# Kernel tuning notes

Measured on AMD Instinct MI355X. Metric: run time of the kernel, lower is better.

Reference implementation:

```python
import jax, jax.numpy as jnp
import numpy as np

DIM = 100
SAMPLE = 12
NEG = -9e15
LRELU = 0.2  # opt.alpha


def _forward(emb, pos_table, w1, w2, glu1_w, glu2_w, glu2_b,
             a0, a1, a2, a3, gw1, gw2, gw3, num_w, mask_item,
             alias_inputs, adj, items, seq_features, adj_all):
    B, L = items.shape
    h = emb[items]  # [B, L, D]

    # ---- LocalAggregator: e_k[b,i,j] = leaky_relu(sum_d h[b,i,d]*h[b,j,d]*a_k[d])
    # (same math as tiling to [B, N*N, D] then matmul with a_k, without the huge intermediate)
    def rel(a):
        return jax.nn.leaky_relu(jnp.einsum('bid,bjd->bij', h, h * a[:, 0]), LRELU)

    alpha = jnp.full((B, L, L), NEG, dtype=h.dtype)
    for k, a in enumerate((a0, a1, a2, a3)):
        alpha = jnp.where(adj == k + 1, rel(a), alpha)
    alpha = jax.nn.softmax(alpha, axis=-1)
    h_local = jnp.einsum('bij,bjd->bid', alpha, h)

    # ---- Global: sample 1-hop neighbors from adj_all / num tables
    nbr_idx = adj_all[items]          # [B, L, S]
    nbr_w = num_w[items]              # [B, L, S]
    nbr_vec = emb[nbr_idx]            # [B, L, S, D]

    # session info (mean of masked seq-feature embeddings)
    item_emb = emb[seq_features] * mask_item[..., None]
    sess = jnp.sum(item_emb, axis=1) / jnp.sum(mask_item, axis=-1, keepdims=True)  # [B, D]
    sess = jnp.broadcast_to(sess[:, None, :], (B, L, DIM))

    # GlobalAggregator with extra_vector
    a_in = jnp.concatenate([sess[:, :, None, :] * nbr_vec, nbr_w[..., None]], axis=-1)  # [B,L,S,D+1]
    att = jax.nn.leaky_relu(a_in @ gw1, LRELU)          # [B, L, S, D]
    att = jax.nn.softmax((att @ gw2)[..., 0], axis=-1)  # [B, L, S]
    agg = jnp.sum(att[..., None] * nbr_vec, axis=-2)    # [B, L, D]
    h_global = jax.nn.relu(jnp.concatenate([h, agg], axis=-1) @ gw3)

    h_comb = h_local + h_global
    seq_hidden = jnp.take_along_axis(h_comb, alias_inputs[..., None], axis=1)  # [B, L, D]

    rmask = mask_item[..., None]
    pos = jnp.broadcast_to(pos_table[:L][None], seq_hidden.shape)
    hs = jnp.sum(seq_hidden * rmask, axis=1) / jnp.sum(rmask, axis=1)  # [B, D]
    nh = jnp.tanh(jnp.concatenate([pos, seq_hidden], axis=-1) @ w1)
    nh = jax.nn.sigmoid(nh @ glu1_w + (hs @ glu2_w + glu2_b)[:, None, :])
    beta = (nh @ w2) * rmask                 # [B, L, 1]
    select = jnp.sum(beta * seq_hidden, 1)   # [B, D]
    score = select @ emb[1:].T               # skip item id 0 (padding)
    return jax.nn.softmax(score, axis=-1)


def setup_inputs():
    key = jax.random.key(0)
    B, L, NN, S, D = 256, 64, 100000, SAMPLE, DIM
    stdv = 1.0 / np.sqrt(D)
    ks = jax.random.split(key, 24)
    u = lambda k, s: jax.random.uniform(k, s, jnp.float32, -stdv, stdv)
    return {
        'emb': u(ks[0], (NN, D)),
        'pos_table': u(ks[1], (200, D)),
        'w1': u(ks[2], (2 * D, D)),
        'w2': u(ks[3], (D, 1)),
        'glu1_w': u(ks[4], (D, D)),
        'glu2_w': u(ks[5], (D, D)),
        'glu2_b': u(ks[6], (D,)),
        'a0': u(ks[7], (D, 1)),
        'a1': u(ks[8], (D, 1)),
        'a2': u(ks[9], (D, 1)),
        'a3': u(ks[10], (D, 1)),
        'gw1': u(ks[11], (D + 1, D)),
        'gw2': u(ks[12], (D, 1)),
        'gw3': u(ks[13], (2 * D, D)),
        'num_w': jax.random.uniform(ks[14], (NN, S), jnp.float32, 0.0, 1.0),
        'mask_item': jnp.ones((B, L), jnp.float32),
        'alias_inputs': jax.random.randint(ks[15], (B, L), 0, L),
        'adj': jax.random.randint(ks[16], (B, L, L), 0, 5),
        'items': jax.random.randint(ks[17], (B, L), 0, NN),
        'seq_features': jax.random.randint(ks[18], (B, L), 0, NN),
        'adj_all': jax.random.randint(ks[19], (NN, S), 0, NN),
    }


def reference(emb, pos_table, w1, w2, glu1_w, glu2_w, glu2_b, a0, a1, a2, a3,
              gw1, gw2, gw3, num_w, mask_item, alias_inputs, adj, items,
              seq_features, adj_all):
    return _forward(emb, pos_table, w1, w2, glu1_w, glu2_w, glu2_b,
                    a0, a1, a2, a3, gw1, gw2, gw3, num_w, mask_item,
                    alias_inputs, adj, items, seq_features, adj_all)
```

## Files before the change

kernel.cpp:

```cpp
#include <hip/hip_runtime.h>
#include <math.h>

#define B 256
#define L 64
#define D 100
#define S 12
#define NN 100000
#define E 99999
#define NEG -9e15f
#define LRELU 0.2f
#define M3A (B*L*S)
#define NT5 782
#define CH 28

__device__ __forceinline__ float lrelu(float x){ return x > 0.f ? x : LRELU*x; }

__global__ void k0_pos(const float* __restrict__ pos, const float* __restrict__ w1,
                       float* __restrict__ pos_part){
    int l = blockIdx.x; int d = threadIdx.x;
    if (d >= D) return;
    float acc = 0.f;
    for (int c = 0; c < D; ++c) acc += pos[l*D+c] * w1[c*D+d];
    pos_part[l*D+d] = acc;
}

__global__ void k1_gather(const float* __restrict__ emb, const int* __restrict__ items,
                          const int* __restrict__ seqf, const float* __restrict__ mask,
                          float* __restrict__ h, float* __restrict__ sess){
    int b = blockIdx.x; int tid = threadIdx.x;
    for (int e = tid; e < L*25; e += blockDim.x){
        int l = e / 25, q = e % 25;
        *(float4*)&h[(long)(b*L+l)*D + q*4] =
            *(const float4*)&emb[(long)items[b*L+l]*D + q*4];
    }
    if (tid < D){
        float acc = 0.f, msum = 0.f;
        for (int l = 0; l < L; ++l){
            float mk = mask[b*L+l];
            acc  += emb[(long)seqf[b*L+l]*D + tid] * mk;
            msum += mk;
        }
        sess[b*D+tid] = acc / msum;
    }
}

__global__ __launch_bounds__(256) void k2_local(const float* __restrict__ h,
                         const int* __restrict__ adj,
                         const float* __restrict__ a0, const float* __restrict__ a1,
                         const float* __restrict__ a2, const float* __restrict__ a3,
                         float* __restrict__ hcomb){
    __shared__ __align__(16) float Hd[L*132];
    __shared__ float Alr[L*66];
    __shared__ __align__(16) float a4s[D*4];
    int tid = threadIdx.x;
    int tx = tid & 15, ty = tid >> 4;
    int b = blockIdx.x;

    for (int t = tid; t < D; t += 256){
        a4s[t*4+0] = a0[t]; a4s[t*4+1] = a1[t]; a4s[t*4+2] = a2[t]; a4s[t*4+3] = a3[t];
    }
    for (int e = tid; e < L*D; e += 256){
        int i = e / D, d = e - i*D;
        Hd[i*132 + d] = h[(long)(b*L+i)*D + d];
    }
    for (int e = tid; e < L*32; e += 256){
        int i = e >> 5, c = D + (e & 31);
        Hd[i*132 + c] = 0.f;
    }
    __syncthreads();

    int ksel[4][4];
    #pragma unroll
    for (int i=0;i<4;++i)
        #pragma unroll
        for (int j=0;j<4;++j)
            ksel[i][j] = adj[((long)b*L + ty*4+i)*L + tx*4+j];

    float e0[4][4]={}, e1[4][4]={}, e2[4][4]={}, e3[4][4]={};
    for (int d = 0; d < D; ++d){
        float4 aw = *(const float4*)&a4s[d*4];
        float hi[4], hj[4];
        #pragma unroll
        for (int i=0;i<4;++i) hi[i] = Hd[(ty*4+i)*132 + d];
        #pragma unroll
        for (int j=0;j<4;++j) hj[j] = Hd[(tx*4+j)*132 + d];
        #pragma unroll
        for (int i=0;i<4;++i)
            #pragma unroll
            for (int j=0;j<4;++j){
                float p = hi[i]*hj[j];
                e0[i][j] += p*aw.x;
                e1[i][j] += p*aw.y;
                e2[i][j] += p*aw.z;
                e3[i][j] += p*aw.w;
            }
    }

    #pragma unroll
    for (int i=0;i<4;++i){
        float s[4];
        #pragma unroll
        for (int j=0;j<4;++j){
            int k = ksel[i][j];
            float ev = (k==1) ? e0[i][j] : (k==2) ? e1[i][j]
                     : (k==3) ? e2[i][j] : e3[i][j];
            s[j] = (k>=1 && k<=4) ? lrelu(ev) : NEG;
        }
        float m = fmaxf(fmaxf(s[0],s[1]), fmaxf(s[2],s[3]));
        #pragma unroll
        for (int off=1; off<16; off<<=1) m = fmaxf(m, __shfl_xor(m, off));
        float es[4], sum = 0.f;
        #pragma unroll
        for (int j=0;j<4;++j){ es[j] = expf(s[j]-m); sum += es[j]; }
        #pragma unroll
        for (int off=1; off<16; off<<=1) sum += __shfl_xor(sum, off);
        float inv = 1.f/sum;
        #pragma unroll
        for (int j=0;j<4;++j) Alr[(ty*4+i)*66 + tx*4+j] = es[j]*inv;
    }
    __syncthreads();

    float o[4][8];
    #pragma unroll
    for (int i=0;i<4;++i)
        #pragma unroll
        for (int jj=0;jj<8;++jj) o[i][jj] = 0.f;
    for (int j = 0; j < L; ++j){
        float al[4];
        #pragma unroll
        for (int i=0;i<4;++i) al[i] = Alr[(ty*4+i)*66 + j];
        float4 b0 = *(const float4*)&Hd[j*132 + tx*4];
        float4 b1 = *(const float4*)&Hd[j*132 + 64 + tx*4];
        float bv[8] = {b0.x,b0.y,b0.z,b0.w,b1.x,b1.y,b1.z,b1.w};
        #pragma unroll
        for (int i=0;i<4;++i)
            #pragma unroll
            for (int jj=0;jj<8;++jj) o[i][jj] += al[i]*bv[jj];
    }
    #pragma unroll
    for (int i=0;i<4;++i){
        int row = ty*4+i;
        #pragma unroll
        for (int jj=0;jj<8;++jj){
            int d = (jj<4) ? (tx*4+jj) : (64 + tx*4 + (jj-4));
            if (d < D) hcomb[(long)(b*L+row)*D + d] = o[i][jj];
        }
    }
}

__global__ __launch_bounds__(256) void k3a_logits(const float* __restrict__ emb,
                          const float* __restrict__ sess,
                          const int* __restrict__ items, const int* __restrict__ adj_all,
                          const float* __restrict__ num_w,
                          const float* __restrict__ gw1, const float* __restrict__ gw2,
                          float* __restrict__ att_l){
    __shared__ __align__(16) float As[CH*128];
    __shared__ __align__(16) float Bs[CH*128];
    __shared__ int   idxr[128];
    __shared__ float nbwr[128];
    int tid = threadIdx.x;
    int tx = tid & 15, ty = tid >> 4;
    int r0 = blockIdx.x * 128;
    int b  = r0 / (L*S);

    if (tid < 128){
        int r = r0 + tid;
        int bl = r / S, s = r - bl*S;
        int it = items[bl];
        idxr[tid] = adj_all[it*S + s];
        nbwr[tid] = num_w[it*S + s];
    }
    __syncthreads();

    float acc[8][8];
    #pragma unroll
    for (int i=0;i<8;++i)
        #pragma unroll
        for (int j=0;j<8;++j) acc[i][j] = 0.f;

    for (int chunk = 0; chunk < 4; ++chunk){
        int c0 = chunk*CH;
        for (int e = tid; e < 128*7; e += 256){
            int rl = e & 127, cq = e >> 7;
            int cb = c0 + cq*4;
            float vx=0.f, vy=0.f, vz=0.f, vw=0.f;
            if (cb < D){
                const float4 v  = *(const float4*)&emb[(long)idxr[rl]*D + cb];
                const float4 sv = *(const float4*)&sess[(long)b*D + cb];
                vx = v.x*sv.x; vy = v.y*sv.y; vz = v.z*sv.z; vw = v.w*sv.w;
            } else if (cb == D){
                vx = nbwr[rl];
            }
            As[(cq*4+0)*128 + rl] = vx;
            As[(cq*4+1)*128 + rl] = vy;
            As[(cq*4+2)*128 + rl] = vz;
            As[(cq*4+3)*128 + rl] = vw;
        }
        for (int e = tid; e < CH*128; e += 256){
            int d = e & 127, cc = e >> 7;
            int c = c0 + cc;
            Bs[cc*128 + d] = (c <= D && d < D) ? gw1[c*D + d] : 0.f;
        }
        __syncthreads();
        for (int k = 0; k < CH; ++k){
            float4 a0v = *(const float4*)&As[k*128 + ty*8];
            float4 a1v = *(const float4*)&As[k*128 + ty*8 + 4];
            float4 b0 = *(const float4*)&Bs[k*128 + tx*4];
            float4 b1 = *(const float4*)&Bs[k*128 + 64 + tx*4];
            float av[8] = {a0v.x,a0v.y,a0v.z,a0v.w,a1v.x,a1v.y,a1v.z,a1v.w};
            float bv[8] = {b0.x,b0.y,b0.z,b0.w,b1.x,b1.y,b1.z,b1.w};
            #pragma unroll
            for (int i=0;i<8;++i)
                #pragma unroll
                for (int j=0;j<8;++j) acc[i][j] += av[i]*bv[j];
        }
        __syncthreads();
    }
    float g[8];
    #pragma unroll
    for (int j=0;j<8;++j){
        int d = (j<4) ? (tx*4+j) : (64 + tx*4 + (j-4));
        g[j] = (d < D) ? gw2[d] : 0.f;
    }
    #pragma unroll
    for (int i=0;i<8;++i){
        float p = 0.f;
        #pragma unroll
        for (int j=0;j<8;++j) p += lrelu(acc[i][j]) * g[j];
        #pragma unroll
        for (int off=1; off<16; off<<=1) p += __shfl_xor(p, off);
        if (tx == 0) att_l[r0 + ty*8 + i] = p;
    }
}

__global__ __launch_bounds__(256) void k3b_agg(const float* __restrict__ emb,
                          const int* __restrict__ items, const int* __restrict__ adj_all,
                          const float* __restrict__ att_l,
                          float* __restrict__ agg){
    int p = blockIdx.x*2 + (threadIdx.x >> 7);
    int t = threadIdx.x & 127;
    float lg[S];
    float m = -INFINITY;
    #pragma unroll
    for (int s=0;s<S;++s){ lg[s] = att_l[p*S + s]; m = fmaxf(m, lg[s]); }
    float sum = 0.f;
    #pragma unroll
    for (int s=0;s<S;++s){ lg[s] = expf(lg[s]-m); sum += lg[s]; }
    float inv = 1.f/sum;
    if (t < D){
        int it = items[p];
        float acc = 0.f;
        #pragma unroll
        for (int s=0;s<S;++s){
            int idx = adj_all[it*S + s];
            acc += lg[s]*inv * emb[(long)idx*D + t];
        }
        agg[p*D + t] = acc;
    }
}

__global__ __launch_bounds__(256) void k3c_hg(const float* __restrict__ h,
                          const float* __restrict__ agg, const float* __restrict__ gw3,
                          float* __restrict__ hcomb){
    __shared__ __align__(16) float As[52*64];
    __shared__ __align__(16) float Bs[52*128];
    int tid = threadIdx.x;
    int tx = tid & 15, ty = tid >> 4;
    int r0 = blockIdx.x * 64;

    float acc[4][8];
    #pragma unroll
    for (int i=0;i<4;++i)
        #pragma unroll
        for (int j=0;j<8;++j) acc[i][j] = 0.f;

    for (int chunk = 0; chunk < 4; ++chunk){
        int c0 = chunk*52;
        for (int e = tid; e < 64*13; e += 256){
            int rl = e & 63, cq = e >> 6;
            int cb = c0 + cq*4;
            float4 v = {0.f,0.f,0.f,0.f};
            if (cb < D)            v = *(const float4*)&h[(long)(r0+rl)*D + cb];
            else if (cb < 2*D)     v = *(const float4*)&agg[(long)(r0+rl)*D + (cb-D)];
            As[(cq*4+0)*64 + rl] = v.x;
            As[(cq*4+1)*64 + rl] = v.y;
            As[(cq*4+2)*64 + rl] = v.z;
            As[(cq*4+3)*64 + rl] = v.w;
        }
        for (int e = tid; e < 52*128; e += 256){
            int d = e & 127, cc = e >> 7;
            int c = c0 + cc;
            Bs[cc*128 + d] = (c < 2*D && d < D) ? gw3[c*D + d] : 0.f;
        }
        __syncthreads();
        for (int k = 0; k < 52; ++k){
            float4 a  = *(const float4*)&As[k*64 + ty*4];
            float4 b0 = *(const float4*)&Bs[k*128 + tx*4];
            float4 b1 = *(const float4*)&Bs[k*128 + 64 + tx*4];
            float av[4] = {a.x,a.y,a.z,a.w};
            float bv[8] = {b0.x,b0.y,b0.z,b0.w,b1.x,b1.y,b1.z,b1.w};
            #pragma unroll
            for (int i=0;i<4;++i)
                #pragma unroll
                for (int j=0;j<8;++j) acc[i][j] += av[i]*bv[j];
        }
        __syncthreads();
    }
    #pragma unroll
    for (int i=0;i<4;++i){
        int r = r0 + ty*4 + i;
        #pragma unroll
        for (int j=0;j<8;++j){
            int d = (j<4) ? (tx*4+j) : (64 + tx*4 + (j-4));
            if (d < D){
                long o = (long)r*D + d;
                hcomb[o] += fmaxf(acc[i][j], 0.f);
            }
        }
    }
}

__global__ __launch_bounds__(128) void k4a_gate(const float* __restrict__ hcomb,
                          const int* __restrict__ alias_in, const float* __restrict__ mask,
                          const float* __restrict__ glu2_w, const float* __restrict__ glu2_b,
                          float* __restrict__ gate){
    int b = blockIdx.x; int tid = threadIdx.x;
    __shared__ float hsl[D];
    __shared__ float mkl[L];
    __shared__ int   al[L];
    if (tid < L){ al[tid] = alias_in[b*L+tid]; mkl[tid] = mask[b*L+tid]; }
    __syncthreads();
    if (tid < D){
        float acc = 0.f, msum = 0.f;
        for (int l = 0; l < L; ++l){
            acc  += hcomb[(long)(b*L + al[l])*D + tid] * mkl[l];
            msum += mkl[l];
        }
        hsl[tid] = acc / msum;
    }
    __syncthreads();
    if (tid < D){
        float g = glu2_b[tid];
        for (int c = 0; c < D; ++c) g += hsl[c]*glu2_w[c*D+tid];
        gate[b*D+tid] = g;
    }
}

__global__ __launch_bounds__(256) void k4b_nh1(const float* __restrict__ hcomb,
                          const int* __restrict__ alias_in,
                          const float* __restrict__ w1, const float* __restrict__ pos_part,
                          float* __restrict__ nh1){
    __shared__ __align__(16) float As[52*64];
    __shared__ __align__(16) float Bs[52*128];
    __shared__ int al[64];
    int tid = threadIdx.x;
    int tx = tid & 15, ty = tid >> 4;
    int b = blockIdx.x;
    int r0 = b * 64;

    if (tid < 64) al[tid] = alias_in[r0 + tid];
    __syncthreads();

    float acc[4][8];
    #pragma unroll
    for (int i=0;i<4;++i)
        #pragma unroll
        for (int j=0;j<8;++j) acc[i][j] = 0.f;

    for (int chunk = 0; chunk < 2; ++chunk){
        int c0 = chunk*52;
        for (int e = tid; e < 64*13; e += 256){
            int rl = e & 63, cq = e >> 6;
            int cb = c0 + cq*4;
            float4 v = {0.f,0.f,0.f,0.f};
            if (cb < D) v = *(const float4*)&hcomb[(long)(r0 + al[rl])*D + cb];
            As[(cq*4+0)*64 + rl] = v.x;
            As[(cq*4+1)*64 + rl] = v.y;
            As[(cq*4+2)*64 + rl] = v.z;
            As[(cq*4+3)*64 + rl] = v.w;
        }
        for (int e = tid; e < 52*128; e += 256){
            int d = e & 127, cc = e >> 7;
            int c = c0 + cc;
            Bs[cc*128 + d] = (c < D && d < D) ? w1[(D+c)*D + d] : 0.f;
        }
        __syncthreads();
        for (int k = 0; k < 52; ++k){
            float4 a  = *(const float4*)&As[k*64 + ty*4];
            float4 b0 = *(const float4*)&Bs[k*128 + tx*4];
            float4 b1 = *(const float4*)&Bs[k*128 + 64 + tx*4];
            float av[4] = {a.x,a.y,a.z,a.w};
            float bv[8] = {b0.x,b0.y,b0.z,b0.w,b1.x,b1.y,b1.z,b1.w};
            #pragma unroll
            for (int i=0;i<4;++i)
                #pragma unroll
                for (int j=0;j<8;++j) acc[i][j] += av[i]*bv[j];
        }
        __syncthreads();
    }
    #pragma unroll
    for (int i=0;i<4;++i){
        int rl = ty*4 + i;
        #pragma unroll
        for (int j=0;j<8;++j){
            int d = (j<4) ? (tx*4+j) : (64 + tx*4 + (j-4));
            if (d < D){
                float v = tanhf(acc[i][j] + pos_part[rl*D + d]);
                nh1[(long)(r0+rl)*D + d] = v;
            }
        }
    }
}

__global__ __launch_bounds__(256) void k4c_select(const float* __restrict__ nh1,
                          const float* __restrict__ hcomb, const int* __restrict__ alias_in,
                          const float* __restrict__ glu1_w, const float* __restrict__ gate,
                          const float* __restrict__ w2, const float* __restrict__ mask,
                          float* __restrict__ sel_out){
    __shared__ __align__(16) float As[104*64];
    __shared__ __align__(16) float Bs[52*128];
    __shared__ __align__(16) float Ss[64*D];
    __shared__ float red[16*128];
    __shared__ float w2l[128];
    __shared__ float mkl[64];
    __shared__ int   al[64];
    int tid = threadIdx.x;
    int tx = tid & 15, ty = tid >> 4;
    int b = blockIdx.x;
    int r0 = b * 64;

    if (tid < 64){ al[tid] = alias_in[r0 + tid]; mkl[tid] = mask[r0 + tid]; }
    if (tid < 128) w2l[tid] = (tid < D) ? w2[tid] : 0.f;
    __syncthreads();

    for (int e = tid; e < 64*26; e += 256){
        int rl = e & 63, cq = e >> 6;
        int cb = cq*4;
        float4 v = {0.f,0.f,0.f,0.f};
        if (cb < D) v = *(const float4*)&nh1[(long)(r0+rl)*D + cb];
        As[(cb+0)*64 + rl] = v.x;
        As[(cb+1)*64 + rl] = v.y;
        As[(cb+2)*64 + rl] = v.z;
        As[(cb+3)*64 + rl] = v.w;
    }
    for (int e = tid; e < 64*25; e += 256){
        int rl = e / 25, q = e % 25;
        *(float4*)&Ss[rl*D + q*4] = *(const float4*)&hcomb[(long)(r0 + al[rl])*D + q*4];
    }

    float acc[4][8];
    #pragma unroll
    for (int i=0;i<4;++i)
        #pragma unroll
        for (int j=0;j<8;++j) acc[i][j] = 0.f;

    for (int chunk = 0; chunk < 2; ++chunk){
        int c0 = chunk*52;
        __syncthreads();
        for (int e = tid; e < 52*128; e += 256){
            int d = e & 127, cc = e >> 7;
            int c = c0 + cc;
            Bs[cc*128 + d] = (c < D && d < D) ? glu1_w[c*D + d] : 0.f;
        }
        __syncthreads();
        for (int k = 0; k < 52; ++k){
            float4 a  = *(const float4*)&As[(c0+k)*64 + ty*4];
            float4 b0 = *(const float4*)&Bs[k*128 + tx*4];
            float4 b1 = *(const float4*)&Bs[k*128 + 64 + tx*4];
            float av[4] = {a.x,a.y,a.z,a.w};
            float bv[8] = {b0.x,b0.y,b0.z,b0.w,b1.x,b1.y,b1.z,b1.w};
            #pragma unroll
            for (int i=0;i<4;++i)
                #pragma unroll
                for (int j=0;j<8;++j) acc[i][j] += av[i]*bv[j];
        }
    }
    __syncthreads();

    float gl[8];
    #pragma unroll
    for (int j=0;j<8;++j){
        int d = (j<4) ? (tx*4+j) : (64 + tx*4 + (j-4));
        gl[j] = (d < D) ? gate[b*D + d] : 0.f;
    }
    float sp[8];
    #pragma unroll
    for (int j=0;j<8;++j) sp[j] = 0.f;
    #pragma unroll
    for (int i=0;i<4;++i){
        int rl = ty*4 + i;
        float p = 0.f;
        #pragma unroll
        for (int j=0;j<8;++j){
            int d = (j<4) ? (tx*4+j) : (64 + tx*4 + (j-4));
            float z = acc[i][j] + gl[j];
            float nh2 = 1.f/(1.f+expf(-z));
            p += nh2 * w2l[d];
        }
        #pragma unroll
        for (int off=1; off<16; off<<=1) p += __shfl_xor(p, off);
        float beta = p * mkl[rl];
        #pragma unroll
        for (int j=0;j<8;++j){
            int d = (j<4) ? (tx*4+j) : (64 + tx*4 + (j-4));
            if (d < D) sp[j] += beta * Ss[rl*D + d];
        }
    }
    #pragma unroll
    for (int j=0;j<8;++j){
        int d = (j<4) ? (tx*4+j) : (64 + tx*4 + (j-4));
        red[ty*128 + d] = sp[j];
    }
    __syncthreads();
    if (tid < 128){
        float s = 0.f;
        #pragma unroll
        for (int g=0; g<16; ++g) s += red[g*128 + tid];
        if (tid < D) sel_out[b*D + tid] = s;
    }
}

__global__ __launch_bounds__(256) void k5_score(const float* __restrict__ emb,
                                                const float* __restrict__ sel,
                                                float* __restrict__ out,
                                                float* __restrict__ pstats){
    __shared__ __align__(16) float As[CH*128];
    __shared__ __align__(16) float Bs[CH*128];
    int tid = threadIdx.x;
    int tx = tid & 15, ty = tid >> 4;
    int n0 = blockIdx.x * 128;
    int m0 = blockIdx.y * 128;

    float acc[8][8];
    #pragma unroll
    for (int i=0;i<8;++i)
        #pragma unroll
        for (int j=0;j<8;++j) acc[i][j] = 0.f;

    for (int chunk = 0; chunk < 4; ++chunk){
        int c0 = chunk*CH;
        for (int e = tid; e < 128*7; e += 256){
            int rl = e & 127, cq = e >> 7;
            int cb = c0 + cq*4;
            float4 v = {0.f,0.f,0.f,0.f};
            if (cb < D) v = *(const float4*)&sel[(long)(m0+rl)*D + cb];
            As[(cq*4+0)*128 + rl] = v.x;
            As[(cq*4+1)*128 + rl] = v.y;
            As[(cq*4+2)*128 + rl] = v.z;
            As[(cq*4+3)*128 + rl] = v.w;
        }
        for (int e = tid; e < 128*7; e += 256){
            int nl = e & 127, cq = e >> 7;
            int cb = c0 + cq*4;
            int n = n0 + nl;
            float4 v = {0.f,0.f,0.f,0.f};
            if (cb < D && n < E) v = *(const float4*)&emb[(long)(1+n)*D + cb];
            Bs[(cq*4+0)*128 + nl] = v.x;
            Bs[(cq*4+1)*128 + nl] = v.y;
            Bs[(cq*4+2)*128 + nl] = v.z;
            Bs[(cq*4+3)*128 + nl] = v.w;
        }
        __syncthreads();
        for (int k = 0; k < CH; ++k){
            float4 a0v = *(const float4*)&As[k*128 + ty*8];
            float4 a1v = *(const float4*)&As[k*128 + ty*8 + 4];
            float4 b0 = *(const float4*)&Bs[k*128 + tx*4];
            float4 b1 = *(const float4*)&Bs[k*128 + 64 + tx*4];
            float av[8] = {a0v.x,a0v.y,a0v.z,a0v.w,a1v.x,a1v.y,a1v.z,a1v.w};
            float bv[8] = {b0.x,b0.y,b0.z,b0.w,b1.x,b1.y,b1.z,b1.w};
            #pragma unroll
            for (int i=0;i<8;++i)
                #pragma unroll
                for (int j=0;j<8;++j) acc[i][j] += av[i]*bv[j];
        }
        __syncthreads();
    }
    bool fullTile = (n0 + 128 <= E);
    #pragma unroll
    for (int i=0;i<8;++i){
        int m = m0 + ty*8 + i;
        long rowo = (long)m*E;
        if (fullTile){
            *(float4*)&out[rowo + n0 + tx*4]      = *(float4*)&acc[i][0];
            *(float4*)&out[rowo + n0 + 64 + tx*4] = *(float4*)&acc[i][4];
        } else {
            #pragma unroll
            for (int j=0;j<8;++j){
                int n = n0 + ((j<4) ? (tx*4+j) : (64 + tx*4 + (j-4)));
                if (n < E) out[rowo + n] = acc[i][j];
            }
        }
        float mx = -INFINITY, sm = 0.f;
        #pragma unroll
        for (int j=0;j<8;++j){
            int n = n0 + ((j<4) ? (tx*4+j) : (64 + tx*4 + (j-4)));
            if (n < E){
                float v = acc[i][j];
                if (v > mx){ sm = sm*expf(mx - v) + 1.f; mx = v; }
                else         sm += expf(v - mx);
            }
        }
        #pragma unroll
        for (int off=1; off<16; off<<=1){
            float mo = __shfl_xor(mx, off);
            float so = __shfl_xor(sm, off);
            float mm = fmaxf(mx, mo);
            float sn = 0.f;
            if (mx > -INFINITY) sn += sm*expf(mx-mm);
            if (mo > -INFINITY) sn += so*expf(mo-mm);
            mx = mm; sm = sn;
        }
        if (tx == 0){
            long o = ((long)m*NT5 + blockIdx.x)*2;
            pstats[o] = mx; pstats[o+1] = sm;
        }
    }
}

__global__ __launch_bounds__(256) void k7_combine(const float* __restrict__ pstats,
                                                  float* __restrict__ MS){
    int row = blockIdx.x;
    int tid = threadIdx.x;
    float m = -INFINITY, s = 0.f;
    for (int t = tid; t < NT5; t += 256){
        long o = ((long)row*NT5 + t)*2;
        float m2 = pstats[o], s2 = pstats[o+1];
        float mm = fmaxf(m, m2);
        float sn = 0.f;
        if (m  > -INFINITY) sn += s *expf(m -mm);
        if (m2 > -INFINITY) sn += s2*expf(m2-mm);
        m = mm; s = sn;
    }
    __shared__ float ms[256], ss[256];
    ms[tid] = m; ss[tid] = s;
    __syncthreads();
    for (int off = 128; off >= 1; off >>= 1){
        if (tid < off){
            float m1 = ms[tid], s1 = ss[tid];
            float m2 = ms[tid+off], s2 = ss[tid+off];
            float mm = fmaxf(m1, m2);
            float sn = 0.f;
            if (m1 > -INFINITY) sn += s1*expf(m1-mm);
            if (m2 > -INFINITY) sn += s2*expf(m2-mm);
            ms[tid] = mm; ss[tid] = sn;
        }
        __syncthreads();
    }
    if (tid == 0){ MS[row*2] = ms[0]; MS[row*2+1] = 1.f/ss[0]; }
}

__global__ __launch_bounds__(256) void k8_norm(float* __restrict__ out,
                                               const float* __restrict__ MS){
    long base = ((long)blockIdx.x*256 + threadIdx.x)*4;
    const long total = (long)B*E;
    if (base < total){
        float4 v = *(float4*)&out[base];
        float r[4] = {v.x, v.y, v.z, v.w};
        #pragma unroll
        for (int c=0;c<4;++c){
            long el = base + c;
            int b = (int)(el / E);
            r[c] = expf(r[c] - MS[b*2]) * MS[b*2+1];
        }
        v.x = r[0]; v.y = r[1]; v.z = r[2]; v.w = r[3];
        *(float4*)&out[base] = v;
    }
}

extern "C" void kernel_launch(void* const* d_in, const int* in_sizes, int n_in,
                              void* d_out, int out_size, void* d_ws, size_t ws_size,
                              hipStream_t stream) {
    const float* emb       = (const float*)d_in[0];
    const float* pos_table = (const float*)d_in[1];
    const float* w1        = (const float*)d_in[2];
    const float* w2        = (const float*)d_in[3];
    const float* glu1_w    = (const float*)d_in[4];
    const float* glu2_w    = (const float*)d_in[5];
    const float* glu2_b    = (const float*)d_in[6];
    const float* a0        = (const float*)d_in[7];
    const float* a1        = (const float*)d_in[8];
    const float* a2        = (const float*)d_in[9];
    const float* a3        = (const float*)d_in[10];
    const float* gw1       = (const float*)d_in[11];
    const float* gw2       = (const float*)d_in[12];
    const float* gw3       = (const float*)d_in[13];
    const float* num_w     = (const float*)d_in[14];
    const float* mask      = (const float*)d_in[15];
    const int*   alias_in  = (const int*)d_in[16];
    const int*   adj       = (const int*)d_in[17];
    const int*   items     = (const int*)d_in[18];
    const int*   seqf      = (const int*)d_in[19];
    const int*   adj_all   = (const int*)d_in[20];

    float* ws       = (float*)d_ws;
    float* h        = ws;
    float* hcomb    = h + B*L*D;
    float* sess     = hcomb + B*L*D;
    float* pos_part = sess + B*D;
    float* sel      = pos_part + L*D;
    float* att_l    = sel + B*D;
    float* agg      = att_l + M3A;
    float* pstats   = agg + B*L*D;
    float* MS       = pstats + B*NT5*2;
    float* gate     = MS + B*2;
    float* nh1      = agg;

    float* out = (float*)d_out;

    k0_pos    <<<dim3(L), dim3(128), 0, stream>>>(pos_table, w1, pos_part);
    k1_gather <<<dim3(B), dim3(128), 0, stream>>>(emb, items, seqf, mask, h, sess);
    k2_local  <<<dim3(B), dim3(256), 0, stream>>>(h, adj, a0, a1, a2, a3, hcomb);
    k3a_logits<<<dim3(M3A/128), dim3(256), 0, stream>>>(emb, sess, items, adj_all, num_w,
                                                        gw1, gw2, att_l);
    k3b_agg   <<<dim3(B*L/2), dim3(256), 0, stream>>>(emb, items, adj_all, att_l, agg);
    k3c_hg    <<<dim3(B*L/64), dim3(256), 0, stream>>>(h, agg, gw3, hcomb);
    k4a_gate  <<<dim3(B), dim3(128), 0, stream>>>(hcomb, alias_in, mask, glu2_w, glu2_b, gate);
    k4b_nh1   <<<dim3(B), dim3(256), 0, stream>>>(hcomb, alias_in, w1, pos_part, nh1);
    k4c_select<<<dim3(B), dim3(256), 0, stream>>>(nh1, hcomb, alias_in, glu1_w, gate,
                                                  w2, mask, sel);
    k5_score  <<<dim3(NT5, 2), dim3(256), 0, stream>>>(emb, sel, out, pstats);
    k7_combine<<<dim3(B), dim3(256), 0, stream>>>(pstats, MS);
    k8_norm   <<<dim3((B*E/4 + 255)/256, 1), dim3(256), 0, stream>>>(out, MS);
}
```

Measured before the change: 622.7 us.

## Retile score GEMM to wide item tiles with transposed session vectors read directly

The k4c_select kernel now also writes a transposed, zero-padded copy of the session vectors. The score kernel reads A operands for its 8 rows straight from that copy in global memory (broadcast within a wavefront) instead of staging them in shared memory. Each block now covers 256 items × 32 rows with 8×4 register tiles, and the grid grows to 8 row blocks. The aim is to raise occupancy through smaller register and shared-memory footprints and to stream the 400MB output better. The cost is that each embedding tile is reloaded 8 times instead of twice, and A operands now come from global loads.

```diff
diff --git a/kernel.cpp b/kernel.cpp
--- a/kernel.cpp
+++ b/kernel.cpp
@@ -10,7 +10,7 @@
 #define NEG -9e15f
 #define LRELU 0.2f
 #define M3A (B*L*S)
-#define NT5 782
+#define NT5 391
 #define CH 28
 
 __device__ __forceinline__ float lrelu(float x){ return x > 0.f ? x : LRELU*x; }
@@ -416,7 +416,7 @@
                           const float* __restrict__ hcomb, const int* __restrict__ alias_in,
                           const float* __restrict__ glu1_w, const float* __restrict__ gate,
                           const float* __restrict__ w2, const float* __restrict__ mask,
-                          float* __restrict__ sel_out){
+                          float* __restrict__ sel_out, float* __restrict__ selT){
     __shared__ __align__(16) float As[104*64];
     __shared__ __align__(16) float Bs[52*128];
     __shared__ __align__(16) float Ss[64*D];
@@ -516,92 +516,81 @@
         float s = 0.f;
         #pragma unroll
         for (int g=0; g<16; ++g) s += red[g*128 + tid];
-        if (tid < D) sel_out[b*D + tid] = s;
+        if (tid < D){
+            sel_out[b*D + tid] = s;
+            selT[(long)tid*256 + b] = s;
+        } else if (tid < 112){
+            selT[(long)tid*256 + b] = 0.f;
+        }
     }
 }
 
 __global__ __launch_bounds__(256) void k5_score(const float* __restrict__ emb,
-                                                const float* __restrict__ sel,
+                                                const float* __restrict__ selT,
                                                 float* __restrict__ out,
                                                 float* __restrict__ pstats){
-    __shared__ __align__(16) float As[CH*128];
-    __shared__ __align__(16) float Bs[CH*128];
+    __shared__ __align__(16) float Bs[CH*256];
     int tid = threadIdx.x;
-    int tx = tid & 15, ty = tid >> 4;
-    int n0 = blockIdx.x * 128;
-    int m0 = blockIdx.y * 128;
-
-    float acc[8][8];
+    int wid = tid >> 6, lane = tid & 63;
+    int n0 = blockIdx.x * 256;
+    int r0 = blockIdx.y * 32 + wid * 8;
+
+    float acc[8][4];
     #pragma unroll
     for (int i=0;i<8;++i)
         #pragma unroll
-        for (int j=0;j<8;++j) acc[i][j] = 0.f;
+        for (int j=0;j<4;++j) acc[i][j] = 0.f;
 
     for (int chunk = 0; chunk < 4; ++chunk){
         int c0 = chunk*CH;
-        for (int e = tid; e < 128*7; e += 256){
-            int rl = e & 127, cq = e >> 7;
-            int cb = c0 + cq*4;
-            float4 v = {0.f,0.f,0.f,0.f};
-            if (cb < D) v = *(const float4*)&sel[(long)(m0+rl)*D + cb];
-            As[(cq*4+0)*128 + rl] = v.x;
-            As[(cq*4+1)*128 + rl] = v.y;
-            As[(cq*4+2)*128 + rl] = v.z;
-            As[(cq*4+3)*128 + rl] = v.w;
-        }
-        for (int e = tid; e < 128*7; e += 256){
-            int nl = e & 127, cq = e >> 7;
-            int cb = c0 + cq*4;
-            int n = n0 + nl;
+        for (int e = tid; e < 256*7; e += 256){
+            int col = e & 255, kq = e >> 8;
+            int cb = c0 + kq*4;
+            int n = n0 + col;
             float4 v = {0.f,0.f,0.f,0.f};
             if (cb < D && n < E) v = *(const float4*)&emb[(long)(1+n)*D + cb];
-            Bs[(cq*4+0)*128 + nl] = v.x;
-            Bs[(cq*4+1)*128 + nl] = v.y;
-            Bs[(cq*4+2)*128 + nl] = v.z;
-            Bs[(cq*4+3)*128 + nl] = v.w;
+            Bs[(kq*4+0)*256 + col] = v.x;
+            Bs[(kq*4+1)*256 + col] = v.y;
+            Bs[(kq*4+2)*256 + col] = v.z;
+            Bs[(kq*4+3)*256 + col] = v.w;
         }
         __syncthreads();
         for (int k = 0; k < CH; ++k){
-            float4 a0v = *(const float4*)&As[k*128 + ty*8];
-            float4 a1v = *(const float4*)&As[k*128 + ty*8 + 4];
-            float4 b0 = *(const float4*)&Bs[k*128 + tx*4];
-            float4 b1 = *(const float4*)&Bs[k*128 + 64 + tx*4];
-            float av[8] = {a0v.x,a0v.y,a0v.z,a0v.w,a1v.x,a1v.y,a1v.z,a1v.w};
-            float bv[8] = {b0.x,b0.y,b0.z,b0.w,b1.x,b1.y,b1.z,b1.w};
+            float4 a0 = *(const float4*)&selT[(long)(c0+k)*256 + r0];
+            float4 a1 = *(const float4*)&selT[(long)(c0+k)*256 + r0 + 4];
+            float4 bv4 = *(const float4*)&Bs[k*256 + lane*4];
+            float av[8] = {a0.x,a0.y,a0.z,a0.w,a1.x,a1.y,a1.z,a1.w};
+            float bv[4] = {bv4.x,bv4.y,bv4.z,bv4.w};
             #pragma unroll
             for (int i=0;i<8;++i)
                 #pragma unroll
-                for (int j=0;j<8;++j) acc[i][j] += av[i]*bv[j];
-        }
-        __syncthreads();
-    }
-    bool fullTile = (n0 + 128 <= E);
+                for (int j=0;j<4;++j) acc[i][j] += av[i]*bv[j];
+        }
+        __syncthreads();
+    }
+    int nbase = n0 + lane*4;
+    bool full4 = (nbase + 4 <= E);
     #pragma unroll
     for (int i=0;i<8;++i){
-        int m = m0 + ty*8 + i;
+        int m = r0 + i;
         long rowo = (long)m*E;
-        if (fullTile){
-            *(float4*)&out[rowo + n0 + tx*4]      = *(float4*)&acc[i][0];
-            *(float4*)&out[rowo + n0 + 64 + tx*4] = *(float4*)&acc[i][4];
+        if (full4){
+            *(float4*)&out[rowo + nbase] = *(float4*)&acc[i][0];
         } else {
             #pragma unroll
-            for (int j=0;j<8;++j){
-                int n = n0 + ((j<4) ? (tx*4+j) : (64 + tx*4 + (j-4)));
-                if (n < E) out[rowo + n] = acc[i][j];
-            }
+            for (int j=0;j<4;++j) if (nbase+j < E) out[rowo + nbase + j] = acc[i][j];
         }
         float mx = -INFINITY, sm = 0.f;
         #pragma unroll
-        for (int j=0;j<8;++j){
-            int n = n0 + ((j<4) ? (tx*4+j) : (64 + tx*4 + (j-4)));
-            if (n < E){
+        for (int j=0;j<4;++j){
+            if (nbase + j < E){
                 float v = acc[i][j];
                 if (v > mx){ sm = sm*expf(mx - v) + 1.f; mx = v; }
                 else         sm += expf(v - mx);
             }
         }
         #pragma unroll
-        for (int off=1; off<16; off<<=1){
+        for (int off=1; off<64; off<<=1){
             float mo = __shfl_xor(mx, off);
             float so = __shfl_xor(sm, off);
             float mm = fmaxf(mx, mo);
@@ -610,7 +599,7 @@
             if (mo > -INFINITY) sn += so*expf(mo-mm);
             mx = mm; sm = sn;
         }
-        if (tx == 0){
+        if (lane == 0){
             long o = ((long)m*NT5 + blockIdx.x)*2;
             pstats[o] = mx; pstats[o+1] = sm;
         }
@@ -698,7 +687,8 @@
     float* sess     = hcomb + B*L*D;
     float* pos_part = sess + B*D;
     float* sel      = pos_part + L*D;
-    float* att_l    = sel + B*D;
+    float* selT     = sel + B*D;
+    float* att_l    = selT + 112*256;
     float* agg      = att_l + M3A;
     float* pstats   = agg + B*L*D;
     float* MS       = pstats + B*NT5*2;
@@ -717,8 +707,8 @@
     k4a_gate  <<<dim3(B), dim3(128), 0, stream>>>(hcomb, alias_in, mask, glu2_w, glu2_b, gate);
     k4b_nh1   <<<dim3(B), dim3(256), 0, stream>>>(hcomb, alias_in, w1, pos_part, nh1);
     k4c_select<<<dim3(B), dim3(256), 0, stream>>>(nh1, hcomb, alias_in, glu1_w, gate,
-                                                  w2, mask, sel);
-    k5_score  <<<dim3(NT5, 2), dim3(256), 0, stream>>>(emb, sel, out, pstats);
+                                                  w2, mask, sel, selT);
+    k5_score  <<<dim3(NT5, 8), dim3(256), 0, stream>>>(emb, selT, out, pstats);
     k7_combine<<<dim3(B), dim3(256), 0, stream>>>(pstats, MS);
     k8_norm   <<<dim3((B*E/4 + 255)/256, 1), dim3(256), 0, stream>>>(out, MS);
 }
```

After: 829.1 us. 1.33x slower.
